# Optimization experiments

Measured on AMD Instinct MI355X. Metric: run time of the kernel, lower is better.

Reference implementation:

```python
import jax, jax.numpy as jnp
import numpy as np

KM_ITERS = 20  # fixed Lloyd iterations (scipy kmeans iterates to tolerance with random init;
               # we use deterministic min/max init so centroid 0 = dark, 1 = bright)


def _kmeans_mask(img2d):
    """2-means clustering of pixel intensities of one [H,W] image + border-vote flip."""
    H, W = img2d.shape
    x = img2d.reshape(-1)  # [N]
    c0 = jnp.stack([x.min(), x.max()])  # deterministic init: centroid0=min, centroid1=max

    def step(c, _):
        code = jnp.argmin(jnp.abs(x[:, None] - c[None, :]), axis=1)  # [N] in {0,1}
        one = code == 1
        n1 = jnp.sum(one)
        n0 = x.shape[0] - n1
        s1 = jnp.sum(jnp.where(one, x, jnp.zeros_like(x)))
        s0 = jnp.sum(x) - s1
        c_new = jnp.stack([s0 / jnp.maximum(n0, 1).astype(x.dtype),
                           s1 / jnp.maximum(n1, 1).astype(x.dtype)])
        return c_new, None

    c, _ = jax.lax.scan(step, c0, None, length=KM_ITERS)
    # final assignment (scipy vq step)
    code = jnp.argmin(jnp.abs(x[:, None] - c[None, :]), axis=1).reshape(H, W)

    # border vote: if >=3 borders are mostly cluster-1, flip so text region is 1
    fc = code[:, 0].sum()
    lc = code[:, -1].sum()
    fr = code[0, :].sum()
    lr = code[-1, :].sum()
    num = ((fr > W // 2).astype(jnp.int32) + (lr > W // 2).astype(jnp.int32)
           + (fc > H // 2).astype(jnp.int32) + (lc > H // 2).astype(jnp.int32))
    mask = jnp.where(num >= 3, 1 - code, code)
    return mask.astype(img2d.dtype)


def get_mask(img_tensor):
    gray = img_tensor.mean(axis=1)  # [B,H,W]
    # clustering is non-differentiable in the original (runs on detached CPU numpy)
    masks = jax.vmap(_kmeans_mask)(jax.lax.stop_gradient(gray))
    return masks[:, None, :, :]  # [B,1,H,W]


def setup_inputs() -> dict:
    key = jax.random.key(0)
    k1, k2 = jax.random.split(key)
    B, C, H, W = 128, 3, 256, 256
    hr_img = jax.random.uniform(k1, (B, C, H, W), dtype=jnp.float32)
    sr_mask = jax.random.uniform(k2, (B, 1, H, W), dtype=jnp.float32)
    return {"hr_img": hr_img, "sr_mask": sr_mask}


def reference(hr_img, sr_mask):
    hr_mask = get_mask(hr_img)  # same spatial size -> no interpolation branch
    return jnp.mean((sr_mask - hr_mask) ** 2)
```

## Files before the change

kernel.cpp:

```cpp
#include <hip/hip_runtime.h>


constexpr int NB   = 2048;
constexpr int NPIX = 65536;
constexpr int KM_ITERS = 20;
constexpr float QINV = 1.0f / 65536.0f;
constexpr float BINW = 1.0f / 2048.0f;

constexpr size_t OFF_MMN = 0;
constexpr size_t OFF_MMX = 4096;
constexpr size_t OFF_SR2 = 8192;
constexpr size_t OFF_ACC = 12288;
constexpr size_t OFF_BG  = 16384;
constexpr size_t OFF_CNT = OFF_BG + 262144;
constexpr size_t OFF_SV  = OFF_CNT + 8388608;

__device__ __forceinline__ float waveSumF(float v) {
#pragma unroll
    for (int off = 32; off > 0; off >>= 1) v += __shfl_down(v, off, 64);
    return v;
}
__device__ __forceinline__ unsigned waveMinU(unsigned v) {
#pragma unroll
    for (int off = 32; off > 0; off >>= 1) v = min(v, (unsigned)__shfl_down((int)v, off, 64));
    return v;
}
__device__ __forceinline__ unsigned waveMaxU(unsigned v) {
#pragma unroll
    for (int off = 32; off > 0; off >>= 1) v = max(v, (unsigned)__shfl_down((int)v, off, 64));
    return v;
}

__global__ __launch_bounds__(256) void kA_hist(
        const float* __restrict__ hr, const float* __restrict__ sr,
        unsigned* __restrict__ mmn, unsigned* __restrict__ mmx,
        float* __restrict__ bsr2, ushort* __restrict__ bg,
        unsigned* __restrict__ cslab, float* __restrict__ vslab,
        float* __restrict__ acc, unsigned* __restrict__ done) {
    const int blk = blockIdx.x, img = blk >> 3, part = blk & 7;
    const int tid = threadIdx.x, lane = tid & 63, wid = tid >> 6;

    __shared__ unsigned hc[NB];
    __shared__ float    hv[NB];
    __shared__ unsigned smn[4], smx[4];
    __shared__ float    ssq[4];
    for (int j = tid; j < NB; j += 256) { hc[j] = 0u; hv[j] = 0.0f; }
    if (blk == 0 && tid == 0) { *acc = 0.0f; *done = 0u; }
    __syncthreads();

    const float* rr = hr + (size_t)img * 3 * NPIX;
    const float* gg = rr + NPIX;
    const float* bb = gg + NPIX;
    const float* sp = sr + (size_t)img * NPIX;
    ushort* bgp = bg + (size_t)img * 1024;

    unsigned umn = 65535u, umx = 0u;
    float sq = 0.0f;
#pragma unroll
    for (int i = 0; i < 8; ++i) {
        const int p = part * 8192 + i * 1024 + tid * 4;
        float4 r4 = *(const float4*)(rr + p);
        float4 g4 = *(const float4*)(gg + p);
        float4 b4 = *(const float4*)(bb + p);
        float4 s4 = *(const float4*)(sp + p);
        const float x[4] = { (r4.x + g4.x + b4.x) * (1.0f / 3.0f),
                             (r4.y + g4.y + b4.y) * (1.0f / 3.0f),
                             (r4.z + g4.z + b4.z) * (1.0f / 3.0f),
                             (r4.w + g4.w + b4.w) * (1.0f / 3.0f) };
        const float sv[4] = { s4.x, s4.y, s4.z, s4.w };
        unsigned u[4];
#pragma unroll
        for (int j = 0; j < 4; ++j) {
            unsigned uu = (unsigned)(x[j] * 65536.0f);
            uu = min(uu, 65535u);
            u[j] = uu;
            umn = min(umn, uu); umx = max(umx, uu);
            atomicAdd(&hc[uu >> 5], 1u);
            atomicAdd(&hv[uu >> 5], sv[j]);
            sq += sv[j] * sv[j];
        }
        const int row = p >> 8, colb = p & 255;
        if (row == 0) {
            ushort4 q; q.x = (ushort)u[0]; q.y = (ushort)u[1];
            q.z = (ushort)u[2]; q.w = (ushort)u[3];
            *(ushort4*)(bgp + colb) = q;
        }
        if (row == 255) {
            ushort4 q; q.x = (ushort)u[0]; q.y = (ushort)u[1];
            q.z = (ushort)u[2]; q.w = (ushort)u[3];
            *(ushort4*)(bgp + 256 + colb) = q;
        }
        if (colb == 0)   bgp[512 + row] = (ushort)u[0];
        if (colb == 252) bgp[768 + row] = (ushort)u[3];
    }
    __syncthreads();

    for (int j = tid; j < NB; j += 256) {
        cslab[(size_t)blk * NB + j] = hc[j];
        vslab[(size_t)blk * NB + j] = hv[j];
    }

    sq = waveSumF(sq); umn = waveMinU(umn); umx = waveMaxU(umx);
    if (lane == 0) { ssq[wid] = sq; smn[wid] = umn; smx[wid] = umx; }
    __syncthreads();
    if (tid == 0) {
        bsr2[blk] = ssq[0] + ssq[1] + ssq[2] + ssq[3];
        mmn[blk] = min(min(smn[0], smn[1]), min(smn[2], smn[3]));
        mmx[blk] = max(max(smx[0], smx[1]), max(smx[2], smx[3]));
    }
}

__global__ __launch_bounds__(256) void kB_all(
        const unsigned* __restrict__ mmn, const unsigned* __restrict__ mmx,
        const float* __restrict__ bsr2, const ushort* __restrict__ bg,
        const unsigned* __restrict__ cslab, const float* __restrict__ vslab,
        float* __restrict__ acc, unsigned* __restrict__ done,
        float* __restrict__ out) {
    const int img = blockIdx.x, tid = threadIdx.x;
    const int lane = tid & 63, wid = tid >> 6;
    __shared__ float sN[NB + 1], sS[NB + 1], sV[NB + 1];
    __shared__ float tN[256], tS[256], tV[256];
    __shared__ float bres[4];
    __shared__ float4 sB4[4];

    const int base = tid * 8;
    unsigned aC[8] = {0u,0u,0u,0u,0u,0u,0u,0u};
    float    aV[8] = {0.f,0.f,0.f,0.f,0.f,0.f,0.f,0.f};
#pragma unroll
    for (int s = 0; s < 8; ++s) {
        const unsigned* cp = cslab + (size_t)(img * 8 + s) * NB + base;
        const float*    vp = vslab + (size_t)(img * 8 + s) * NB + base;
        const uint4  c0 = *(const uint4*)cp;
        const uint4  c1 = *(const uint4*)(cp + 4);
        const float4 v0 = *(const float4*)vp;
        const float4 v1 = *(const float4*)(vp + 4);
        aC[0] += c0.x; aC[1] += c0.y; aC[2] += c0.z; aC[3] += c0.w;
        aC[4] += c1.x; aC[5] += c1.y; aC[6] += c1.z; aC[7] += c1.w;
        aV[0] += v0.x; aV[1] += v0.y; aV[2] += v0.z; aV[3] += v0.w;
        aV[4] += v1.x; aV[5] += v1.y; aV[6] += v1.z; aV[7] += v1.w;
    }

    float n8[8], s8[8], v8[8];
#pragma unroll
    for (int u = 0; u < 8; ++u) {
        const float c = (float)aC[u];
        n8[u] = c;
        s8[u] = c * (((float)(base + u) + 0.484375f) * BINW);
        v8[u] = aV[u];
    }
    float accN = 0.0f, accS = 0.0f, accV = 0.0f;
#pragma unroll
    for (int u = 7; u >= 0; --u) {
        accN += n8[u]; n8[u] = accN;
        accS += s8[u]; s8[u] = accS;
        accV += v8[u]; v8[u] = accV;
    }
    tN[tid] = accN; tS[tid] = accS; tV[tid] = accV;
    __syncthreads();
    for (int off = 1; off < 256; off <<= 1) {
        float aNN = 0.0f, aSS = 0.0f, aVV = 0.0f;
        if (tid + off < 256) { aNN = tN[tid + off]; aSS = tS[tid + off]; aVV = tV[tid + off]; }
        __syncthreads();
        tN[tid] += aNN; tS[tid] += aSS; tV[tid] += aVV;
        __syncthreads();
    }
    const float exN = (tid < 255) ? tN[tid + 1] : 0.0f;
    const float exS = (tid < 255) ? tS[tid + 1] : 0.0f;
    const float exV = (tid < 255) ? tV[tid + 1] : 0.0f;
#pragma unroll
    for (int u = 0; u < 8; ++u) {
        sN[base + u] = n8[u] + exN;
        sS[base + u] = s8[u] + exS;
        sV[base + u] = v8[u] + exV;
    }
    if (tid == 0) { sN[NB] = 0.0f; sS[NB] = 0.0f; sV[NB] = 0.0f; }
    __syncthreads();

    if (tid == 0) {
        unsigned bmn = 65535u, bmx = 0u;
#pragma unroll
        for (int s = 0; s < 8; ++s) {
            bmn = min(bmn, mmn[img * 8 + s]);
            bmx = max(bmx, mmx[img * 8 + s]);
        }
        float c0 = (float)bmn * QINV;
        float c1 = (float)bmx * QINV;
        const float Stot = sS[0];
        const float Ntot = (float)NPIX;
#pragma unroll 1
        for (int it = 0; it < KM_ITERS; ++it) {
            const float t = 0.5f * (c0 + c1);
            float n1, s1;
            if (c1 == c0) { n1 = 0.0f; s1 = 0.0f; }
            else {
                const float f = t * (float)NB;
                int k = (int)floorf(f);
                k = max(0, min(NB - 1, k));
                float frac = (float)(k + 1) - f;
                frac = fminf(fmaxf(frac, 0.0f), 1.0f);
                const float cntk = sN[k] - sN[k + 1];
                const float aNt = sN[k + 1] + cntk * frac;
                const float aSt = sS[k + 1] +
                                  cntk * frac * 0.5f * (t + (float)(k + 1) * BINW);
                if (c1 > c0) { n1 = aNt; s1 = aSt; }
                else         { n1 = Ntot - aNt; s1 = Stot - aSt; }
            }
            const float c1n = s1 / fmaxf(n1, 1.0f);
            const float c0n = (Stot - s1) / fmaxf(Ntot - n1, 1.0f);
            if (c1n == c1 && c0n == c0) break;
            c0 = c0n; c1 = c1n;
        }

        float Sr2 = 0.0f;
#pragma unroll
        for (int s = 0; s < 8; ++s) Sr2 += bsr2[img * 8 + s];
        const float SvTot = sV[0];

        float tf, hii, n1, s1v;
        if (c1 == c0) { tf = -1e30f; hii = 0.0f; n1 = 0.0f; s1v = 0.0f; }
        else {
            tf = 0.5f * (c0 + c1);
            const float f = tf * (float)NB;
            int k = (int)floorf(f);
            k = max(0, min(NB - 1, k));
            float frac = (float)(k + 1) - f;
            frac = fminf(fmaxf(frac, 0.0f), 1.0f);
            const float cntk = sN[k] - sN[k + 1];
            const float aNt = sN[k + 1] + cntk * frac;
            const float svk = sV[k] - sV[k + 1];
            const float aSv = sV[k + 1] + svk * frac;
            if (c1 > c0) { hii = 1.0f; n1 = aNt;        s1v = aSv; }
            else         { hii = 0.0f; n1 = Ntot - aNt; s1v = SvTot - aSv; }
        }
        bres[0] = tf; bres[1] = hii;
        bres[2] = Sr2 - 2.0f * s1v + n1;
        bres[3] = Sr2 - 2.0f * (SvTot - s1v) + (Ntot - n1);
    }
    __syncthreads();

    const float tf = bres[0];
    const bool hi = (bres[1] != 0.0f);
    const ushort* bp = bg + (size_t)img * 1024;
    const float x0 = (float)bp[tid]       * QINV;
    const float x1 = (float)bp[256 + tid] * QINV;
    const float x2 = (float)bp[512 + tid] * QINV;
    const float x3 = (float)bp[768 + tid] * QINV;
    float fr = (hi ? (x0 > tf) : (x0 < tf)) ? 1.0f : 0.0f;
    float lr = (hi ? (x1 > tf) : (x1 < tf)) ? 1.0f : 0.0f;
    float fc = (hi ? (x2 > tf) : (x2 < tf)) ? 1.0f : 0.0f;
    float lc = (hi ? (x3 > tf) : (x3 < tf)) ? 1.0f : 0.0f;
    fr = waveSumF(fr); lr = waveSumF(lr); fc = waveSumF(fc); lc = waveSumF(lc);
    if (lane == 0) sB4[wid] = make_float4(fr, lr, fc, lc);
    __syncthreads();
    if (tid == 0) {
        const float FR = sB4[0].x + sB4[1].x + sB4[2].x + sB4[3].x;
        const float LR = sB4[0].y + sB4[1].y + sB4[2].y + sB4[3].y;
        const float FC = sB4[0].z + sB4[1].z + sB4[2].z + sB4[3].z;
        const float LC = sB4[0].w + sB4[1].w + sB4[2].w + sB4[3].w;
        const int num = (FR > 128.0f) + (LR > 128.0f) + (FC > 128.0f) + (LC > 128.0f);
        const float chosen = (num >= 3) ? bres[3] : bres[2];
        atomicAdd(acc, chosen);
        __threadfence();
        const unsigned old = atomicAdd(done, 1u);
        if (old == 127u) {
            const float tot = atomicAdd(acc, 0.0f);
            out[0] = tot * (1.0f / 8388608.0f);
        }
    }
}

extern "C" void kernel_launch(void* const* d_in, const int* in_sizes, int n_in,
                              void* d_out, int out_size, void* d_ws, size_t ws_size,
                              hipStream_t stream) {
    const float* hr = (const float*)d_in[0];
    const float* sr = (const float*)d_in[1];
    float* out = (float*)d_out;

    char* ws = (char*)d_ws;
    unsigned* mmn   = (unsigned*)(ws + OFF_MMN);
    unsigned* mmx   = (unsigned*)(ws + OFF_MMX);
    float*    bsr2  = (float*)(ws + OFF_SR2);
    float*    acc   = (float*)(ws + OFF_ACC);
    unsigned* done  = (unsigned*)(ws + OFF_ACC + 4);
    ushort*   bg    = (ushort*)(ws + OFF_BG);
    unsigned* cslab = (unsigned*)(ws + OFF_CNT);
    float*    vslab = (float*)(ws + OFF_SV);

    kA_hist<<<1024, 256, 0, stream>>>(hr, sr, mmn, mmx, bsr2, bg, cslab, vslab, acc, done);
    kB_all <<< 128, 256, 0, stream>>>(mmn, mmx, bsr2, bg, cslab, vslab, acc, done, out);
}
```

Before: 189.1 us.

## Pack count and fixed-point sum into 64-bit histogram bins with global atomics

Replaces the separate per-block count and float-sum histograms with one 64-bit LDS histogram per block, whose bins hold the count in the high bits and a 24-bit fixed-point sr sum in the low bits. One atomic per pixel then does the work of two. Blocks merge into a per-image global histogram with 64-bit global atomics instead of writing 8 slabs that kB reads back. Block size doubles to 512 and a memset is added to zero the histogram. The fixed-point quantisation of sr changes the sums slightly from the float version.

```diff
diff --git a/kernel.cpp b/kernel.cpp
--- a/kernel.cpp
+++ b/kernel.cpp
@@ -6,14 +6,16 @@
 constexpr int KM_ITERS = 20;
 constexpr float QINV = 1.0f / 65536.0f;
 constexpr float BINW = 1.0f / 2048.0f;
-
-constexpr size_t OFF_MMN = 0;
-constexpr size_t OFF_MMX = 4096;
-constexpr size_t OFF_SR2 = 8192;
-constexpr size_t OFF_ACC = 12288;
-constexpr size_t OFF_BG  = 16384;
-constexpr size_t OFF_CNT = OFF_BG + 262144;
-constexpr size_t OFF_SV  = OFF_CNT + 8388608;
+constexpr unsigned long long CNT1   = 1ull << 40;
+constexpr unsigned long long SVMASK = CNT1 - 1;
+
+constexpr size_t OFF_HIST = 0;
+constexpr size_t OFF_MMN  = 2097152;
+constexpr size_t OFF_MMX  = OFF_MMN + 4096;
+constexpr size_t OFF_SR2  = OFF_MMX + 4096;
+constexpr size_t OFF_ACC  = OFF_SR2 + 4096;
+constexpr size_t OFF_BG   = OFF_ACC + 4096;
+constexpr size_t MEMSET_BYTES = 2097152;
 
 __device__ __forceinline__ float waveSumF(float v) {
 #pragma unroll
@@ -31,20 +33,19 @@
     return v;
 }
 
-__global__ __launch_bounds__(256) void kA_hist(
+__global__ __launch_bounds__(512) void kA_hist(
         const float* __restrict__ hr, const float* __restrict__ sr,
+        unsigned long long* __restrict__ hist,
         unsigned* __restrict__ mmn, unsigned* __restrict__ mmx,
         float* __restrict__ bsr2, ushort* __restrict__ bg,
-        unsigned* __restrict__ cslab, float* __restrict__ vslab,
         float* __restrict__ acc, unsigned* __restrict__ done) {
     const int blk = blockIdx.x, img = blk >> 3, part = blk & 7;
     const int tid = threadIdx.x, lane = tid & 63, wid = tid >> 6;
 
-    __shared__ unsigned hc[NB];
-    __shared__ float    hv[NB];
-    __shared__ unsigned smn[4], smx[4];
-    __shared__ float    ssq[4];
-    for (int j = tid; j < NB; j += 256) { hc[j] = 0u; hv[j] = 0.0f; }
+    __shared__ unsigned long long h64[NB];
+    __shared__ unsigned smn[8], smx[8];
+    __shared__ float    ssq[8];
+    for (int j = tid; j < NB; j += 512) h64[j] = 0ull;
     if (blk == 0 && tid == 0) { *acc = 0.0f; *done = 0u; }
     __syncthreads();
 
@@ -57,8 +58,8 @@
     unsigned umn = 65535u, umx = 0u;
     float sq = 0.0f;
 #pragma unroll
-    for (int i = 0; i < 8; ++i) {
-        const int p = part * 8192 + i * 1024 + tid * 4;
+    for (int i = 0; i < 4; ++i) {
+        const int p = part * 8192 + i * 2048 + tid * 4;
         float4 r4 = *(const float4*)(rr + p);
         float4 g4 = *(const float4*)(gg + p);
         float4 b4 = *(const float4*)(bb + p);
@@ -75,45 +76,50 @@
             uu = min(uu, 65535u);
             u[j] = uu;
             umn = min(umn, uu); umx = max(umx, uu);
-            atomicAdd(&hc[uu >> 5], 1u);
-            atomicAdd(&hv[uu >> 5], sv[j]);
+            unsigned q = (unsigned)(sv[j] * 16777216.0f);
+            q = min(q, 16777215u);
+            atomicAdd(&h64[uu >> 5], CNT1 + (unsigned long long)q);
             sq += sv[j] * sv[j];
         }
         const int row = p >> 8, colb = p & 255;
         if (row == 0) {
-            ushort4 q; q.x = (ushort)u[0]; q.y = (ushort)u[1];
-            q.z = (ushort)u[2]; q.w = (ushort)u[3];
-            *(ushort4*)(bgp + colb) = q;
+            ushort4 qq; qq.x = (ushort)u[0]; qq.y = (ushort)u[1];
+            qq.z = (ushort)u[2]; qq.w = (ushort)u[3];
+            *(ushort4*)(bgp + colb) = qq;
         }
         if (row == 255) {
-            ushort4 q; q.x = (ushort)u[0]; q.y = (ushort)u[1];
-            q.z = (ushort)u[2]; q.w = (ushort)u[3];
-            *(ushort4*)(bgp + 256 + colb) = q;
+            ushort4 qq; qq.x = (ushort)u[0]; qq.y = (ushort)u[1];
+            qq.z = (ushort)u[2]; qq.w = (ushort)u[3];
+            *(ushort4*)(bgp + 256 + colb) = qq;
         }
         if (colb == 0)   bgp[512 + row] = (ushort)u[0];
         if (colb == 252) bgp[768 + row] = (ushort)u[3];
     }
     __syncthreads();
 
-    for (int j = tid; j < NB; j += 256) {
-        cslab[(size_t)blk * NB + j] = hc[j];
-        vslab[(size_t)blk * NB + j] = hv[j];
+    unsigned long long* gh = hist + (size_t)img * NB;
+    for (int j = tid; j < NB; j += 512) {
+        const unsigned long long v = h64[j];
+        if (v) atomicAdd(&gh[j], v);
     }
 
     sq = waveSumF(sq); umn = waveMinU(umn); umx = waveMaxU(umx);
     if (lane == 0) { ssq[wid] = sq; smn[wid] = umn; smx[wid] = umx; }
     __syncthreads();
     if (tid == 0) {
-        bsr2[blk] = ssq[0] + ssq[1] + ssq[2] + ssq[3];
-        mmn[blk] = min(min(smn[0], smn[1]), min(smn[2], smn[3]));
-        mmx[blk] = max(max(smx[0], smx[1]), max(smx[2], smx[3]));
+        float SQ = 0.0f; unsigned MN = 65535u, MX = 0u;
+#pragma unroll
+        for (int w = 0; w < 8; ++w) {
+            SQ += ssq[w]; MN = min(MN, smn[w]); MX = max(MX, smx[w]);
+        }
+        bsr2[blk] = SQ; mmn[blk] = MN; mmx[blk] = MX;
     }
 }
 
 __global__ __launch_bounds__(256) void kB_all(
         const unsigned* __restrict__ mmn, const unsigned* __restrict__ mmx,
         const float* __restrict__ bsr2, const ushort* __restrict__ bg,
-        const unsigned* __restrict__ cslab, const float* __restrict__ vslab,
+        const unsigned long long* __restrict__ hist,
         float* __restrict__ acc, unsigned* __restrict__ done,
         float* __restrict__ out) {
     const int img = blockIdx.x, tid = threadIdx.x;
@@ -124,30 +130,22 @@
     __shared__ float4 sB4[4];
 
     const int base = tid * 8;
-    unsigned aC[8] = {0u,0u,0u,0u,0u,0u,0u,0u};
-    float    aV[8] = {0.f,0.f,0.f,0.f,0.f,0.f,0.f,0.f};
-#pragma unroll
-    for (int s = 0; s < 8; ++s) {
-        const unsigned* cp = cslab + (size_t)(img * 8 + s) * NB + base;
-        const float*    vp = vslab + (size_t)(img * 8 + s) * NB + base;
-        const uint4  c0 = *(const uint4*)cp;
-        const uint4  c1 = *(const uint4*)(cp + 4);
-        const float4 v0 = *(const float4*)vp;
-        const float4 v1 = *(const float4*)(vp + 4);
-        aC[0] += c0.x; aC[1] += c0.y; aC[2] += c0.z; aC[3] += c0.w;
-        aC[4] += c1.x; aC[5] += c1.y; aC[6] += c1.z; aC[7] += c1.w;
-        aV[0] += v0.x; aV[1] += v0.y; aV[2] += v0.z; aV[3] += v0.w;
-        aV[4] += v1.x; aV[5] += v1.y; aV[6] += v1.z; aV[7] += v1.w;
-    }
-
+    const unsigned long long* gh = hist + (size_t)img * NB + base;
     float n8[8], s8[8], v8[8];
 #pragma unroll
-    for (int u = 0; u < 8; ++u) {
-        const float c = (float)aC[u];
-        n8[u] = c;
-        s8[u] = c * (((float)(base + u) + 0.484375f) * BINW);
-        v8[u] = aV[u];
-    }
+    for (int u2 = 0; u2 < 4; ++u2) {
+        const ulonglong2 vv = *(const ulonglong2*)(gh + u2 * 2);
+        const unsigned long long va = vv.x, vb = vv.y;
+        const float ca = (float)(unsigned)(va >> 40);
+        const float cb = (float)(unsigned)(vb >> 40);
+        n8[u2 * 2]     = ca;
+        n8[u2 * 2 + 1] = cb;
+        s8[u2 * 2]     = ca * (((float)(base + u2 * 2)     + 0.484375f) * BINW);
+        s8[u2 * 2 + 1] = cb * (((float)(base + u2 * 2 + 1) + 0.484375f) * BINW);
+        v8[u2 * 2]     = (float)(va & SVMASK) * (1.0f / 16777216.0f);
+        v8[u2 * 2 + 1] = (float)(vb & SVMASK) * (1.0f / 16777216.0f);
+    }
+
     float accN = 0.0f, accS = 0.0f, accV = 0.0f;
 #pragma unroll
     for (int u = 7; u >= 0; --u) {
@@ -277,15 +275,15 @@
     float* out = (float*)d_out;
 
     char* ws = (char*)d_ws;
-    unsigned* mmn   = (unsigned*)(ws + OFF_MMN);
-    unsigned* mmx   = (unsigned*)(ws + OFF_MMX);
-    float*    bsr2  = (float*)(ws + OFF_SR2);
-    float*    acc   = (float*)(ws + OFF_ACC);
-    unsigned* done  = (unsigned*)(ws + OFF_ACC + 4);
-    ushort*   bg    = (ushort*)(ws + OFF_BG);
-    unsigned* cslab = (unsigned*)(ws + OFF_CNT);
-    float*    vslab = (float*)(ws + OFF_SV);
-
-    kA_hist<<<1024, 256, 0, stream>>>(hr, sr, mmn, mmx, bsr2, bg, cslab, vslab, acc, done);
-    kB_all <<< 128, 256, 0, stream>>>(mmn, mmx, bsr2, bg, cslab, vslab, acc, done, out);
-}
+    unsigned long long* hist = (unsigned long long*)(ws + OFF_HIST);
+    unsigned* mmn  = (unsigned*)(ws + OFF_MMN);
+    unsigned* mmx  = (unsigned*)(ws + OFF_MMX);
+    float*    bsr2 = (float*)(ws + OFF_SR2);
+    float*    acc  = (float*)(ws + OFF_ACC);
+    unsigned* done = (unsigned*)(ws + OFF_ACC + 4);
+    ushort*   bg   = (ushort*)(ws + OFF_BG);
+
+    hipMemsetAsync(hist, 0, MEMSET_BYTES, stream);
+    kA_hist<<<1024, 512, 0, stream>>>(hr, sr, hist, mmn, mmx, bsr2, bg, acc, done);
+    kB_all <<< 128, 256, 0, stream>>>(mmn, mmx, bsr2, bg, hist, acc, done, out);
+}
```

After: 186.4 us. No clear change (-1.4%).
